# Performance work log

Hardware: AMD Instinct MI355X
Metric: run time of the kernel (lower is better)

The kernel has to match this reference:

```python
import jax, jax.numpy as jnp
import numpy as np

D_MODEL = 512
STATE = 128
HALF = STATE // 2
SEQ = 4096
BATCH = 8


def setup_inputs() -> dict:
    key = jax.random.key(0)
    ks = jax.random.split(key, 4)
    u = jax.random.normal(ks[0], (BATCH, SEQ, D_MODEL), dtype=jnp.float32)
    # HiPPO init: Lambda = -0.5 + i*pi*n, n=1..HALF
    n = jnp.arange(1, HALF + 1, dtype=jnp.float32)
    log_Lambda_real = jnp.log(jnp.full((HALF,), 0.5, dtype=jnp.float32))  # log(-real) with real=-0.5
    Lambda_imag = jnp.pi * n
    B_real = jnp.ones((HALF, D_MODEL), dtype=jnp.float32)
    B_imag = jnp.zeros((HALF, D_MODEL), dtype=jnp.float32)
    C_real = jax.random.normal(ks[1], (D_MODEL, HALF), dtype=jnp.float32) / np.sqrt(STATE)
    C_imag = jax.random.normal(ks[2], (D_MODEL, HALF), dtype=jnp.float32) / np.sqrt(STATE)
    D = jax.random.normal(ks[3], (D_MODEL, D_MODEL), dtype=jnp.float32) / np.sqrt(D_MODEL)
    log_Delta = jnp.array([-3.0], dtype=jnp.float32)
    return {
        "u": u,
        "log_Lambda_real": log_Lambda_real,
        "Lambda_imag": Lambda_imag,
        "B_real": B_real,
        "B_imag": B_imag,
        "C_real": C_real,
        "C_imag": C_imag,
        "D": D,
        "log_Delta": log_Delta,
    }


def reference(u, log_Lambda_real, Lambda_imag, B_real, B_imag, C_real, C_imag, D, log_Delta):
    T = u.shape[1]
    Bc = B_real + 1j * B_imag            # (N/2, P) complex
    Cc = C_real + 1j * C_imag            # (P, N/2) complex
    # --- bilinear (Tustin) discretization ---
    Delta = jnp.exp(log_Delta)           # (1,)
    Lambda = -jnp.exp(jnp.clip(log_Lambda_real, -10.0, 10.0)) + 1j * Lambda_imag  # (N/2,)
    denom = 1.0 - (Delta / 2.0) * Lambda
    A_bar = (1.0 + (Delta / 2.0) * Lambda) / denom          # (N/2,)
    B_bar = (Delta / denom)[:, None] * Bc                   # (N/2, P)
    # --- FFT convolution with the SSM kernel k[n,t] = A_bar[n]^t ---
    t_idx = jnp.arange(T)
    k = jnp.exp(jnp.log(A_bar)[:, None] * t_idx[None, :])   # (N/2, T)
    u_c = u.astype(jnp.complex64)
    v = jnp.einsum('np,btp->bnt', B_bar, u_c)               # (B, N/2, T)
    fft_size = 2 * T
    V_f = jnp.fft.fft(v, n=fft_size, axis=-1)
    K_f = jnp.fft.fft(k, n=fft_size, axis=-1)
    conv = jnp.fft.ifft(V_f * K_f[None, :, :], axis=-1)[..., :T]  # (B, N/2, T)
    y = 2.0 * jnp.einsum('pn,bnt->btp', Cc, conv).real      # (B, T, P)
    return y + u @ D.T
```

## Files before the change

### kernel.cpp

```cpp
#include <hip/hip_runtime.h>
#include <hip/hip_bf16.h>
#include <stdint.h>


#define BATCH 8
#define SEQ   4096
#define DMODEL 512
#define HALF  64
#define CHUNK 64
#define NCHUNK (SEQ / CHUNK)
#define NT    10

typedef __attribute__((ext_vector_type(8))) short short8;
typedef __attribute__((ext_vector_type(4))) float f32x4;

__device__ __forceinline__ unsigned short f2bf(float f) {
    unsigned int u = __float_as_uint(f);
    u += 0x7fffu + ((u >> 16) & 1u);
    return (unsigned short)(u >> 16);
}
__device__ __forceinline__ float bf2f(unsigned short s) {
    return __uint_as_float((unsigned)s << 16);
}

#define GLOAD_LDS16(g, l)                                                    \
    __builtin_amdgcn_global_load_lds(                                        \
        (const __attribute__((address_space(1))) unsigned int*)(g),          \
        (__attribute__((address_space(3))) unsigned int*)(l), 16, 0, 0)


__global__ void k_consts(const float* __restrict__ logLr,
                         const float* __restrict__ Li_in,
                         const float* __restrict__ logDelta,
                         float* __restrict__ sr, float* __restrict__ si,
                         float* __restrict__ ApR, float* __restrict__ ApI) {
    int n = threadIdx.x;
    float Delta = expf(logDelta[0]);
    float llr = fminf(fmaxf(logLr[n], -10.f), 10.f);
    float Lr = -expf(llr);
    float Li = Li_in[n];
    float dr = 1.f - 0.5f * Delta * Lr;
    float di = -0.5f * Delta * Li;
    float dn = dr * dr + di * di;
    float nr = 1.f + 0.5f * Delta * Lr;
    float ni = 0.5f * Delta * Li;
    float Ar = (nr * dr + ni * di) / dn;
    float Ai = (ni * dr - nr * di) / dn;
    sr[n] = Delta * dr / dn;
    si[n] = -Delta * di / dn;
    float pr = 1.f, pi = 0.f;
    for (int k = 0; k <= CHUNK; ++k) {
        ApR[k * HALF + n] = pr;
        ApI[k * HALF + n] = pi;
        float npr = pr * Ar - pi * Ai;
        float npi = pr * Ai + pi * Ar;
        pr = npr; pi = npi;
    }
}

__global__ void k_build_Mv(const float* __restrict__ Br, const float* __restrict__ Bi,
                           const float* __restrict__ sr, const float* __restrict__ si,
                           unsigned short* __restrict__ Mv) {
    int np = blockIdx.x, p = threadIdx.x;
    int n = np & 63;
    float br = Br[n * DMODEL + p], bi = Bi[n * DMODEL + p];
    float v = (np < HALF) ? (sr[n] * br - si[n] * bi)
                          : (si[n] * br + sr[n] * bi);
    Mv[np * DMODEL + p] = f2bf(v);
}

__global__ void k_build_W(const float* __restrict__ Cr, const float* __restrict__ Ci,
                          const float* __restrict__ D, unsigned short* __restrict__ W) {
    int p = blockIdx.x, j = threadIdx.x;
    float v;
    if (j < HALF) v = 2.f * Cr[p * HALF + j];
    else if (j < 2 * HALF) v = -2.f * Ci[p * HALF + (j - HALF)];
    else v = D[p * DMODEL + (j - 2 * HALF)];
    W[p * 640 + j] = f2bf(v);
}


__global__ void k_scanA(const unsigned short* __restrict__ Vb,
                        const float* __restrict__ ApR, const float* __restrict__ ApI,
                        float* __restrict__ E) {
    int tid = threadIdx.x;
    int n = tid & 63;
    int c = ((blockIdx.x & 31) << 1) + (tid >> 6);
    int b = blockIdx.x >> 5;
    float Ar = ApR[HALF + n], Ai = ApI[HALF + n];
    float xr = 0.f, xi = 0.f;
    size_t base = ((size_t)b * SEQ + (size_t)c * CHUNK) * 128 + n;
    for (int tl = 0; tl < CHUNK; ++tl) {
        float vr = bf2f(Vb[base]), vi = bf2f(Vb[base + 64]);
        float nxr = Ar * xr - Ai * xi + vr;
        float nxi = Ar * xi + Ai * xr + vi;
        xr = nxr; xi = nxi;
        base += 128;
    }
    int eidx = ((b * NCHUNK + c) * 2) * HALF + n;
    E[eidx] = xr; E[eidx + 64] = xi;
}

__global__ void k_scanB(const float* __restrict__ E, float* __restrict__ Carry,
                        const float* __restrict__ ApR, const float* __restrict__ ApI) {
    int lane = threadIdx.x & 63;
    int wv = threadIdx.x >> 6;
    int b = blockIdx.x;
    for (int n = wv; n < HALF; n += 8) {
        float wr = ApR[CHUNK * HALF + n], wi = ApI[CHUNK * HALF + n];
        int idx = ((b * NCHUNK + lane) * 2) * HALF + n;
        float sR = E[idx], sI = E[idx + 64];
#pragma unroll
        for (int s = 1; s < 64; s <<= 1) {
            float pR = __shfl_up(sR, s, 64);
            float pI = __shfl_up(sI, s, 64);
            if (lane >= s) {
                sR += wr * pR - wi * pI;
                sI += wr * pI + wi * pR;
            }
            float nwr = wr * wr - wi * wi;
            float nwi = 2.f * wr * wi;
            wr = nwr; wi = nwi;
        }
        float cR = __shfl_up(sR, 1, 64);
        float cI = __shfl_up(sI, 1, 64);
        if (lane == 0) { cR = 0.f; cI = 0.f; }
        Carry[idx] = cR; Carry[idx + 64] = cI;
    }
}

__global__ void k_scanC(const unsigned short* __restrict__ Vb,
                        const float* __restrict__ Carry,
                        const float* __restrict__ ApR, const float* __restrict__ ApI,
                        unsigned short* __restrict__ Xb) {
    int tid = threadIdx.x;
    int n = tid & 63;
    int c = ((blockIdx.x & 31) << 1) + (tid >> 6);
    int b = blockIdx.x >> 5;
    int cidx = ((b * NCHUNK + c) * 2) * HALF + n;
    float xr = Carry[cidx], xi = Carry[cidx + 64];
    float Ar = ApR[HALF + n], Ai = ApI[HALF + n];
    size_t base = ((size_t)b * SEQ + (size_t)c * CHUNK) * 128 + n;
    for (int tl = 0; tl < CHUNK; ++tl) {
        float vr = bf2f(Vb[base]), vi = bf2f(Vb[base + 64]);
        float nxr = Ar * xr - Ai * xi + vr;
        float nxi = Ar * xi + Ai * xr + vi;
        xr = nxr; xi = nxi;
        Xb[base] = f2bf(xr); Xb[base + 64] = f2bf(xi);
        base += 128;
    }
}

__global__ __launch_bounds__(512) void gemm1(const float* __restrict__ U,
                                             const unsigned short* __restrict__ Mv,
                                             unsigned short* __restrict__ Vb,
                                             unsigned short* __restrict__ Ub) {
    __shared__ __align__(16) unsigned short As[64 * 32];
    __shared__ __align__(16) unsigned short Bs[128 * 32];
    const int tid = threadIdx.x;
    const int lane = tid & 63;
    const int w = tid >> 6;
    const int wm = w >> 2, wn = w & 3;
    const int l15 = lane & 15, l4 = lane >> 4;
    const int row0 = blockIdx.x * 64;
    const int srow = tid >> 3;
    const int sh = (tid & 7) * 4;

    f32x4 acc[2][2];
#pragma unroll
    for (int m = 0; m < 2; ++m)
#pragma unroll
        for (int n = 0; n < 2; ++n) acc[m][n] = (f32x4)(0.f);

    for (int k0 = 0; k0 < DMODEL; k0 += 32) {
        const float4 av = *(const float4*)(U + (size_t)(row0 + srow) * DMODEL + k0 + sh);

        __syncthreads();

        GLOAD_LDS16(Mv + (size_t)(tid >> 2) * DMODEL + k0 + (tid & 3) * 8,
                    &Bs[(w * 64) * 8]);

        uint2 wa;
        wa.x = (unsigned)f2bf(av.x) | ((unsigned)f2bf(av.y) << 16);
        wa.y = (unsigned)f2bf(av.z) | ((unsigned)f2bf(av.w) << 16);
        *(uint2*)&As[srow * 32 + sh] = wa;
        *(uint2*)&Ub[(size_t)(row0 + srow) * DMODEL + k0 + sh] = wa;

        __syncthreads();

        short8 af[2], bf[2];
#pragma unroll
        for (int m = 0; m < 2; ++m)
            af[m] = *(const short8*)&As[(wm * 32 + m * 16 + l15) * 32 + l4 * 8];
#pragma unroll
        for (int n = 0; n < 2; ++n)
            bf[n] = *(const short8*)&Bs[(wn * 32 + n * 16 + l15) * 32 + l4 * 8];
#pragma unroll
        for (int m = 0; m < 2; ++m)
#pragma unroll
            for (int n = 0; n < 2; ++n)
                acc[m][n] = __builtin_amdgcn_mfma_f32_16x16x32_bf16(af[m], bf[n], acc[m][n], 0, 0, 0);
    }

#pragma unroll
    for (int m = 0; m < 2; ++m) {
        int rbase = row0 + wm * 32 + m * 16 + l4 * 4;
#pragma unroll
        for (int n = 0; n < 2; ++n) {
            int col = wn * 32 + n * 16 + l15;
#pragma unroll
            for (int r = 0; r < 4; ++r)
                Vb[(size_t)(rbase + r) * 128 + col] = f2bf(acc[m][n][r]);
        }
    }
}


#define STAGE_K(t, kh, j) do {                                                 \
    int c_ = (kh) * 1024 + (j) * 512 + tid;                                    \
    int ct_ = c_ ^ (((c_ >> 5) & 1) << 1);                                     \
    int r_ = (ct_ >> 2) & 255;                                                 \
    int kcol_ = (t) * 64 + (kh) * 32 + (ct_ & 3) * 8;                          \
    const unsigned short* asrc_ = (kcol_ < 128)                                \
        ? Xb + (size_t)(row0 + r_) * 128 + kcol_                               \
        : Ub + (size_t)(row0 + r_) * 512 + (kcol_ - 128);                      \
    GLOAD_LDS16(asrc_, &As[((t) & 1) * 16384 + ((kh) * 1024 + (j) * 512 + w * 64) * 8]); \
    GLOAD_LDS16(W + (size_t)(col0 + r_) * 640 + kcol_,                         \
                &Bs[((t) & 1) * 16384 + ((kh) * 1024 + (j) * 512 + w * 64) * 8]); \
} while (0)

#define LDAB(t, kh) do {                                                       \
    _Pragma("unroll") for (int i_ = 0; i_ < 8; ++i_) {                         \
        int r_ = wm * 128 + i_ * 16 + l15;                                     \
        int c_ = (l4 * 8) ^ (((r_ >> 3) & 1) << 4);                            \
        af[i_] = *(const short8*)&As[((t) & 1) * 16384 + (kh) * 8192 + r_ * 32 + c_]; \
    }                                                                          \
    _Pragma("unroll") for (int j_ = 0; j_ < 4; ++j_) {                         \
        int r_ = wn * 64 + j_ * 16 + l15;                                      \
        int c_ = (l4 * 8) ^ (((r_ >> 3) & 1) << 4);                            \
        bf[j_] = *(const short8*)&Bs[((t) & 1) * 16384 + (kh) * 8192 + r_ * 32 + c_]; \
    } } while (0)

#define MFMA32() do {                                                          \
    __builtin_amdgcn_s_setprio(1);                                             \
    _Pragma("unroll") for (int i_ = 0; i_ < 8; ++i_)                           \
    _Pragma("unroll") for (int j_ = 0; j_ < 4; ++j_)                           \
        acc[i_][j_] = __builtin_amdgcn_mfma_f32_16x16x32_bf16(                 \
            af[i_], bf[j_], acc[i_][j_], 0, 0, 0);                             \
    __builtin_amdgcn_s_setprio(0);                                             \
} while (0)

#define PHASE_SYNC(N) do {                                                     \
    asm volatile("s_waitcnt vmcnt(" #N ")" ::: "memory");                      \
    __builtin_amdgcn_s_barrier();                                              \
    __builtin_amdgcn_sched_barrier(0);                                         \
} while (0)

__global__ __launch_bounds__(512) void gemm23_8p(const unsigned short* __restrict__ Xb,
                                                 const unsigned short* __restrict__ Ub,
                                                 const unsigned short* __restrict__ W,
                                                 float* __restrict__ C) {
    __shared__ __align__(16) unsigned short As[2 * 16384];
    __shared__ __align__(16) unsigned short Bs[2 * 16384];
    const int tid = threadIdx.x;
    const int lane = tid & 63;
    const int w = tid >> 6;
    const int wm = w >> 2, wn = w & 3;
    const int l15 = lane & 15, l4 = lane >> 4;

    int lin = blockIdx.y * gridDim.x + blockIdx.x;
    int sw = (lin & 7) * 32 + (lin >> 3);
    const int row0 = (sw & 127) * 256;
    const int col0 = (sw >> 7) * 256;

    f32x4 acc[8][4];
#pragma unroll
    for (int m = 0; m < 8; ++m)
#pragma unroll
        for (int n = 0; n < 4; ++n) acc[m][n] = (f32x4)(0.f);

    STAGE_K(0, 0, 0); STAGE_K(0, 0, 1);
    STAGE_K(0, 1, 0); STAGE_K(0, 1, 1);
    STAGE_K(1, 0, 0); STAGE_K(1, 0, 1);

    short8 af[8], bf[4];
    for (int t = 0; t < NT - 1; ++t) {
        PHASE_SYNC(8);
        LDAB(t, 0);
        STAGE_K(t + 1, 1, 0); STAGE_K(t + 1, 1, 1);
        MFMA32();
        PHASE_SYNC(8);
        LDAB(t, 1);
        if (t < NT - 2) { STAGE_K(t + 2, 0, 0); STAGE_K(t + 2, 0, 1); }
        MFMA32();
    }
    PHASE_SYNC(4);
    LDAB(NT - 1, 0);
    MFMA32();
    PHASE_SYNC(0);
    LDAB(NT - 1, 1);
    MFMA32();

#pragma unroll
    for (int m = 0; m < 8; ++m) {
        int rbase = row0 + wm * 128 + m * 16 + l4 * 4;
#pragma unroll
        for (int n = 0; n < 4; ++n) {
            int col = col0 + wn * 64 + n * 16 + l15;
#pragma unroll
            for (int r = 0; r < 4; ++r)
                C[(size_t)(rbase + r) * DMODEL + col] = acc[m][n][r];
        }
    }
}


extern "C" void kernel_launch(void* const* d_in, const int* in_sizes, int n_in,
                              void* d_out, int out_size, void* d_ws, size_t ws_size,
                              hipStream_t stream) {
    const float* u      = (const float*)d_in[0];
    const float* logLr  = (const float*)d_in[1];
    const float* Li     = (const float*)d_in[2];
    const float* Br     = (const float*)d_in[3];
    const float* Bi     = (const float*)d_in[4];
    const float* Cr     = (const float*)d_in[5];
    const float* Ci     = (const float*)d_in[6];
    const float* D      = (const float*)d_in[7];
    const float* logDel = (const float*)d_in[8];
    float* out = (float*)d_out;

    const size_t M = (size_t)BATCH * SEQ;
    unsigned short* Vb = (unsigned short*)d_ws;
    unsigned short* Ub = Vb + M * 128;
    unsigned short* Xb = Ub + M * 512;
    unsigned short* Mv = Xb + M * 128;
    unsigned short* W  = Mv + 128 * 512;
    float* fp    = (float*)(W + 512 * 640);
    float* E     = fp;
    float* Carry = E + 65536;
    float* ApR   = Carry + 65536;
    float* ApI   = ApR + 4160;
    float* sr    = ApI + 4160;
    float* si    = sr + 64;

    hipLaunchKernelGGL(k_consts, dim3(1), dim3(64), 0, stream,
                       logLr, Li, logDel, sr, si, ApR, ApI);
    hipLaunchKernelGGL(k_build_Mv, dim3(128), dim3(512), 0, stream, Br, Bi, sr, si, Mv);
    hipLaunchKernelGGL(k_build_W, dim3(512), dim3(640), 0, stream, Cr, Ci, D, W);

    hipLaunchKernelGGL(gemm1, dim3(M / 64), dim3(512), 0, stream, u, Mv, Vb, Ub);

    hipLaunchKernelGGL(k_scanA, dim3(256), dim3(128), 0, stream, Vb, ApR, ApI, E);
    hipLaunchKernelGGL(k_scanB, dim3(BATCH), dim3(512), 0, stream, E, Carry, ApR, ApI);
    hipLaunchKernelGGL(k_scanC, dim3(256), dim3(128), 0, stream, Vb, Carry, ApR, ApI, Xb);

    hipLaunchKernelGGL(gemm23_8p, dim3(M / 256, DMODEL / 256), dim3(512), 0, stream,
                       Xb, Ub, W, out);
}
```

Before: 85.56 us.

## Fuse local chunk scan into gemm1, make scanC carry-only, retile final GEMM

The first GEMM now stages its output tile in LDS, runs the per-chunk intra-chunk scan there, writes the locally scanned Vb plus chunk end states, and drops the separate scanA kernel. scanC no longer runs a serial recurrence; it adds the carry times precomputed powers of A to the already-scanned values. The final GEMM moves to 128x256 tiles with a 3-stage LDS ring, a vmcnt-based pipeline and a coalesced LDS-staged float4 epilogue. The scan inside gemm1 runs serially on a single wave while the other waves wait, and the ApR/ApI power table must hold A^1..A^64 for the carry formula to be correct.

```diff
diff --git a/kernel.cpp b/kernel.cpp
--- a/kernel.cpp
+++ b/kernel.cpp
@@ -9,7 +9,6 @@
 #define HALF  64
 #define CHUNK 64
 #define NCHUNK (SEQ / CHUNK)
-#define NT    10
 
 typedef __attribute__((ext_vector_type(8))) short short8;
 typedef __attribute__((ext_vector_type(4))) float f32x4;
@@ -79,26 +78,101 @@
     W[p * 640 + j] = f2bf(v);
 }
 
-
-__global__ void k_scanA(const unsigned short* __restrict__ Vb,
-                        const float* __restrict__ ApR, const float* __restrict__ ApI,
-                        float* __restrict__ E) {
-    int tid = threadIdx.x;
-    int n = tid & 63;
-    int c = ((blockIdx.x & 31) << 1) + (tid >> 6);
-    int b = blockIdx.x >> 5;
-    float Ar = ApR[HALF + n], Ai = ApI[HALF + n];
-    float xr = 0.f, xi = 0.f;
-    size_t base = ((size_t)b * SEQ + (size_t)c * CHUNK) * 128 + n;
-    for (int tl = 0; tl < CHUNK; ++tl) {
-        float vr = bf2f(Vb[base]), vi = bf2f(Vb[base + 64]);
-        float nxr = Ar * xr - Ai * xi + vr;
-        float nxi = Ar * xi + Ai * xr + vi;
-        xr = nxr; xi = nxi;
-        base += 128;
-    }
-    int eidx = ((b * NCHUNK + c) * 2) * HALF + n;
-    E[eidx] = xr; E[eidx + 64] = xi;
+__global__ __launch_bounds__(512) void gemm1(const float* __restrict__ U,
+                                             const unsigned short* __restrict__ Mv,
+                                             unsigned short* __restrict__ Vb,
+                                             unsigned short* __restrict__ Ub,
+                                             const float* __restrict__ ApR,
+                                             const float* __restrict__ ApI,
+                                             float* __restrict__ E) {
+    __shared__ __align__(16) unsigned short As[64 * 32];
+    __shared__ __align__(16) unsigned short Bs[128 * 32];
+    __shared__ __align__(16) float Vt[64 * 132];
+    const int tid = threadIdx.x;
+    const int lane = tid & 63;
+    const int w = tid >> 6;
+    const int wm = w >> 2, wn = w & 3;
+    const int l15 = lane & 15, l4 = lane >> 4;
+    const int row0 = blockIdx.x * 64;
+    const int srow = tid >> 3;
+    const int sh = (tid & 7) * 4;
+
+    f32x4 acc[2][2];
+#pragma unroll
+    for (int m = 0; m < 2; ++m)
+#pragma unroll
+        for (int n = 0; n < 2; ++n) acc[m][n] = (f32x4)(0.f);
+
+    for (int k0 = 0; k0 < DMODEL; k0 += 32) {
+        const float4 av = *(const float4*)(U + (size_t)(row0 + srow) * DMODEL + k0 + sh);
+
+        __syncthreads();
+
+        GLOAD_LDS16(Mv + (size_t)(tid >> 2) * DMODEL + k0 + (tid & 3) * 8,
+                    &Bs[(w * 64) * 8]);
+
+        uint2 wa;
+        wa.x = (unsigned)f2bf(av.x) | ((unsigned)f2bf(av.y) << 16);
+        wa.y = (unsigned)f2bf(av.z) | ((unsigned)f2bf(av.w) << 16);
+        *(uint2*)&As[srow * 32 + sh] = wa;
+        *(uint2*)&Ub[(size_t)(row0 + srow) * DMODEL + k0 + sh] = wa;
+
+        __syncthreads();
+
+        short8 af[2], bf[2];
+#pragma unroll
+        for (int m = 0; m < 2; ++m)
+            af[m] = *(const short8*)&As[(wm * 32 + m * 16 + l15) * 32 + l4 * 8];
+#pragma unroll
+        for (int n = 0; n < 2; ++n)
+            bf[n] = *(const short8*)&Bs[(wn * 32 + n * 16 + l15) * 32 + l4 * 8];
+#pragma unroll
+        for (int m = 0; m < 2; ++m)
+#pragma unroll
+            for (int n = 0; n < 2; ++n)
+                acc[m][n] = __builtin_amdgcn_mfma_f32_16x16x32_bf16(af[m], bf[n], acc[m][n], 0, 0, 0);
+    }
+
+    __syncthreads();
+#pragma unroll
+    for (int m = 0; m < 2; ++m)
+#pragma unroll
+        for (int n = 0; n < 2; ++n)
+#pragma unroll
+            for (int r = 0; r < 4; ++r)
+                Vt[(wm * 32 + m * 16 + l4 * 4 + r) * 132 + wn * 32 + n * 16 + l15] = acc[m][n][r];
+    __syncthreads();
+
+    const int b = row0 >> 12;
+    const int c = (row0 >> 6) & 63;
+    if (tid < 64) {
+        int n = tid;
+        float Ar = ApR[HALF + n], Ai = ApI[HALF + n];
+        float xr = 0.f, xi = 0.f;
+        for (int tl = 0; tl < CHUNK; ++tl) {
+            float vr = Vt[tl * 132 + n], vi = Vt[tl * 132 + 64 + n];
+            float nxr = Ar * xr - Ai * xi + vr;
+            float nxi = Ar * xi + Ai * xr + vi;
+            xr = nxr; xi = nxi;
+            Vt[tl * 132 + n] = xr; Vt[tl * 132 + 64 + n] = xi;
+        }
+        int ei = ((b * NCHUNK + c) * 2) * HALF + n;
+        E[ei] = xr; E[ei + 64] = xi;
+    }
+    __syncthreads();
+
+#pragma unroll
+    for (int j = 0; j < 2; ++j) {
+        int idx = tid * 2 + j;
+        int row = idx >> 4, oc = idx & 15;
+        const float* vs = &Vt[row * 132 + oc * 8];
+        uint4 pk;
+        pk.x = (unsigned)f2bf(vs[0]) | ((unsigned)f2bf(vs[1]) << 16);
+        pk.y = (unsigned)f2bf(vs[2]) | ((unsigned)f2bf(vs[3]) << 16);
+        pk.z = (unsigned)f2bf(vs[4]) | ((unsigned)f2bf(vs[5]) << 16);
+        pk.w = (unsigned)f2bf(vs[6]) | ((unsigned)f2bf(vs[7]) << 16);
+        *(uint4*)&Vb[(size_t)(row0 + row) * 128 + oc * 8] = pk;
+    }
 }
 
 __global__ void k_scanB(const float* __restrict__ E, float* __restrict__ Carry,
@@ -138,178 +212,113 @@
     int c = ((blockIdx.x & 31) << 1) + (tid >> 6);
     int b = blockIdx.x >> 5;
     int cidx = ((b * NCHUNK + c) * 2) * HALF + n;
-    float xr = Carry[cidx], xi = Carry[cidx + 64];
-    float Ar = ApR[HALF + n], Ai = ApI[HALF + n];
+    float cr = Carry[cidx], ci = Carry[cidx + 64];
     size_t base = ((size_t)b * SEQ + (size_t)c * CHUNK) * 128 + n;
     for (int tl = 0; tl < CHUNK; ++tl) {
-        float vr = bf2f(Vb[base]), vi = bf2f(Vb[base + 64]);
-        float nxr = Ar * xr - Ai * xi + vr;
-        float nxi = Ar * xi + Ai * xr + vi;
-        xr = nxr; xi = nxi;
+        float pr = ApR[(tl + 1) * HALF + n], pi = ApI[(tl + 1) * HALF + n];
+        float xr = bf2f(Vb[base])      + pr * cr - pi * ci;
+        float xi = bf2f(Vb[base + 64]) + pr * ci + pi * cr;
         Xb[base] = f2bf(xr); Xb[base + 64] = f2bf(xi);
         base += 128;
     }
 }
 
-__global__ __launch_bounds__(512) void gemm1(const float* __restrict__ U,
-                                             const unsigned short* __restrict__ Mv,
-                                             unsigned short* __restrict__ Vb,
-                                             unsigned short* __restrict__ Ub) {
-    __shared__ __align__(16) unsigned short As[64 * 32];
-    __shared__ __align__(16) unsigned short Bs[128 * 32];
+
+#define STAGE_P(p) do {                                                        \
+    const int kb_ = ((p) >> 1) * 64 + ((p) & 1) * 32;                          \
+    { int c_ = tid; int ct_ = c_ ^ (((c_ >> 5) & 1) << 1);                     \
+      int r_ = ct_ >> 2; int kc_ = kb_ + (ct_ & 3) * 8;                        \
+      const unsigned short* s_ = (kc_ < 128)                                   \
+          ? Xb + (size_t)(row0 + r_) * 128 + kc_                               \
+          : Ub + (size_t)(row0 + r_) * 512 + (kc_ - 128);                      \
+      GLOAD_LDS16(s_, &lds[((p) % 3) * 4096 + (w * 64) * 8]); }                \
+    _Pragma("unroll") for (int j_ = 0; j_ < 2; ++j_) {                         \
+      int c_ = j_ * 512 + tid; int ct_ = c_ ^ (((c_ >> 5) & 1) << 1);          \
+      int r_ = ct_ >> 2; int kc_ = kb_ + (ct_ & 3) * 8;                        \
+      GLOAD_LDS16(W + (size_t)(col0 + r_) * 640 + kc_,                         \
+                  &lds[12288 + ((p) % 3) * 8192 + (j_ * 512 + w * 64) * 8]);   \
+    } } while (0)
+
+#define LDAB_P(p) do {                                                         \
+    _Pragma("unroll") for (int i_ = 0; i_ < 4; ++i_) {                         \
+        int r_ = wm * 64 + i_ * 16 + l15;                                      \
+        int c_ = (l4 * 8) ^ (((r_ >> 3) & 1) << 4);                            \
+        af[i_] = *(const short8*)&lds[((p) % 3) * 4096 + r_ * 32 + c_]; }      \
+    _Pragma("unroll") for (int j_ = 0; j_ < 4; ++j_) {                         \
+        int r_ = wn * 64 + j_ * 16 + l15;                                      \
+        int c_ = (l4 * 8) ^ (((r_ >> 3) & 1) << 4);                            \
+        bf[j_] = *(const short8*)&lds[12288 + ((p) % 3) * 8192 + r_ * 32 + c_]; } \
+    } while (0)
+
+#define MFMA16() do {                                                          \
+    __builtin_amdgcn_s_setprio(1);                                             \
+    _Pragma("unroll") for (int i_ = 0; i_ < 4; ++i_)                           \
+    _Pragma("unroll") for (int j_ = 0; j_ < 4; ++j_)                           \
+        acc[i_][j_] = __builtin_amdgcn_mfma_f32_16x16x32_bf16(                 \
+            af[i_], bf[j_], acc[i_][j_], 0, 0, 0);                             \
+    __builtin_amdgcn_s_setprio(0);                                             \
+} while (0)
+
+__global__ __launch_bounds__(512) void gemm23_r(const unsigned short* __restrict__ Xb,
+                                                const unsigned short* __restrict__ Ub,
+                                                const unsigned short* __restrict__ W,
+                                                float* __restrict__ C) {
+    __shared__ __align__(16) unsigned short lds[36864];
     const int tid = threadIdx.x;
     const int lane = tid & 63;
     const int w = tid >> 6;
     const int wm = w >> 2, wn = w & 3;
     const int l15 = lane & 15, l4 = lane >> 4;
-    const int row0 = blockIdx.x * 64;
-    const int srow = tid >> 3;
-    const int sh = (tid & 7) * 4;
-
-    f32x4 acc[2][2];
-#pragma unroll
-    for (int m = 0; m < 2; ++m)
-#pragma unroll
-        for (int n = 0; n < 2; ++n) acc[m][n] = (f32x4)(0.f);
-
-    for (int k0 = 0; k0 < DMODEL; k0 += 32) {
-        const float4 av = *(const float4*)(U + (size_t)(row0 + srow) * DMODEL + k0 + sh);
-
+
+    int lin = blockIdx.y * gridDim.x + blockIdx.x;
+    int sw = (lin & 7) * 64 + (lin >> 3);
+    const int row0 = (sw & 255) * 128;
+    const int col0 = (sw >> 8) * 256;
+
+    f32x4 acc[4][4];
+#pragma unroll
+    for (int m = 0; m < 4; ++m)
+#pragma unroll
+        for (int n = 0; n < 4; ++n) acc[m][n] = (f32x4)(0.f);
+
+    STAGE_P(0);
+    STAGE_P(1);
+
+    short8 af[4], bf[4];
+#pragma unroll
+    for (int p = 0; p < 19; ++p) {
+        asm volatile("s_waitcnt vmcnt(3)" ::: "memory");
+        __builtin_amdgcn_s_barrier();
+        __builtin_amdgcn_sched_barrier(0);
+        LDAB_P(p);
+        if (p < 18) STAGE_P(p + 2);
+        MFMA16();
+    }
+    asm volatile("s_waitcnt vmcnt(0)" ::: "memory");
+    __builtin_amdgcn_s_barrier();
+    __builtin_amdgcn_sched_barrier(0);
+    LDAB_P(19);
+    MFMA16();
+
+    float* lf = (float*)lds;
+#pragma unroll
+    for (int i = 0; i < 4; ++i) {
         __syncthreads();
-
-        GLOAD_LDS16(Mv + (size_t)(tid >> 2) * DMODEL + k0 + (tid & 3) * 8,
-                    &Bs[(w * 64) * 8]);
-
-        uint2 wa;
-        wa.x = (unsigned)f2bf(av.x) | ((unsigned)f2bf(av.y) << 16);
-        wa.y = (unsigned)f2bf(av.z) | ((unsigned)f2bf(av.w) << 16);
-        *(uint2*)&As[srow * 32 + sh] = wa;
-        *(uint2*)&Ub[(size_t)(row0 + srow) * DMODEL + k0 + sh] = wa;
-
+#pragma unroll
+        for (int j = 0; j < 4; ++j)
+#pragma unroll
+            for (int r = 0; r < 4; ++r)
+                lf[(wm * 16 + l4 * 4 + r) * 264 + wn * 64 + j * 16 + l15] = acc[i][j][r];
         __syncthreads();
-
-        short8 af[2], bf[2];
-#pragma unroll
-        for (int m = 0; m < 2; ++m)
-            af[m] = *(const short8*)&As[(wm * 32 + m * 16 + l15) * 32 + l4 * 8];
-#pragma unroll
-        for (int n = 0; n < 2; ++n)
-            bf[n] = *(const short8*)&Bs[(wn * 32 + n * 16 + l15) * 32 + l4 * 8];
-#pragma unroll
-        for (int m = 0; m < 2; ++m)
-#pragma unroll
-            for (int n = 0; n < 2; ++n)
-                acc[m][n] = __builtin_amdgcn_mfma_f32_16x16x32_bf16(af[m], bf[n], acc[m][n], 0, 0, 0);
-    }
-
-#pragma unroll
-    for (int m = 0; m < 2; ++m) {
-        int rbase = row0 + wm * 32 + m * 16 + l4 * 4;
-#pragma unroll
-        for (int n = 0; n < 2; ++n) {
-            int col = wn * 32 + n * 16 + l15;
-#pragma unroll
-            for (int r = 0; r < 4; ++r)
-                Vb[(size_t)(rbase + r) * 128 + col] = f2bf(acc[m][n][r]);
-        }
-    }
-}
-
-
-#define STAGE_K(t, kh, j) do {                                                 \
-    int c_ = (kh) * 1024 + (j) * 512 + tid;                                    \
-    int ct_ = c_ ^ (((c_ >> 5) & 1) << 1);                                     \
-    int r_ = (ct_ >> 2) & 255;                                                 \
-    int kcol_ = (t) * 64 + (kh) * 32 + (ct_ & 3) * 8;                          \
-    const unsigned short* asrc_ = (kcol_ < 128)                                \
-        ? Xb + (size_t)(row0 + r_) * 128 + kcol_                               \
-        : Ub + (size_t)(row0 + r_) * 512 + (kcol_ - 128);                      \
-    GLOAD_LDS16(asrc_, &As[((t) & 1) * 16384 + ((kh) * 1024 + (j) * 512 + w * 64) * 8]); \
-    GLOAD_LDS16(W + (size_t)(col0 + r_) * 640 + kcol_,                         \
-                &Bs[((t) & 1) * 16384 + ((kh) * 1024 + (j) * 512 + w * 64) * 8]); \
-} while (0)
-
-#define LDAB(t, kh) do {                                                       \
-    _Pragma("unroll") for (int i_ = 0; i_ < 8; ++i_) {                         \
-        int r_ = wm * 128 + i_ * 16 + l15;                                     \
-        int c_ = (l4 * 8) ^ (((r_ >> 3) & 1) << 4);                            \
-        af[i_] = *(const short8*)&As[((t) & 1) * 16384 + (kh) * 8192 + r_ * 32 + c_]; \
-    }                                                                          \
-    _Pragma("unroll") for (int j_ = 0; j_ < 4; ++j_) {                         \
-        int r_ = wn * 64 + j_ * 16 + l15;                                      \
-        int c_ = (l4 * 8) ^ (((r_ >> 3) & 1) << 4);                            \
-        bf[j_] = *(const short8*)&Bs[((t) & 1) * 16384 + (kh) * 8192 + r_ * 32 + c_]; \
-    } } while (0)
-
-#define MFMA32() do {                                                          \
-    __builtin_amdgcn_s_setprio(1);                                             \
-    _Pragma("unroll") for (int i_ = 0; i_ < 8; ++i_)                           \
-    _Pragma("unroll") for (int j_ = 0; j_ < 4; ++j_)                           \
-        acc[i_][j_] = __builtin_amdgcn_mfma_f32_16x16x32_bf16(                 \
-            af[i_], bf[j_], acc[i_][j_], 0, 0, 0);                             \
-    __builtin_amdgcn_s_setprio(0);                                             \
-} while (0)
-
-#define PHASE_SYNC(N) do {                                                     \
-    asm volatile("s_waitcnt vmcnt(" #N ")" ::: "memory");                      \
-    __builtin_amdgcn_s_barrier();                                              \
-    __builtin_amdgcn_sched_barrier(0);                                         \
-} while (0)
-
-__global__ __launch_bounds__(512) void gemm23_8p(const unsigned short* __restrict__ Xb,
-                                                 const unsigned short* __restrict__ Ub,
-                                                 const unsigned short* __restrict__ W,
-                                                 float* __restrict__ C) {
-    __shared__ __align__(16) unsigned short As[2 * 16384];
-    __shared__ __align__(16) unsigned short Bs[2 * 16384];
-    const int tid = threadIdx.x;
-    const int lane = tid & 63;
-    const int w = tid >> 6;
-    const int wm = w >> 2, wn = w & 3;
-    const int l15 = lane & 15, l4 = lane >> 4;
-
-    int lin = blockIdx.y * gridDim.x + blockIdx.x;
-    int sw = (lin & 7) * 32 + (lin >> 3);
-    const int row0 = (sw & 127) * 256;
-    const int col0 = (sw >> 7) * 256;
-
-    f32x4 acc[8][4];
-#pragma unroll
-    for (int m = 0; m < 8; ++m)
-#pragma unroll
-        for (int n = 0; n < 4; ++n) acc[m][n] = (f32x4)(0.f);
-
-    STAGE_K(0, 0, 0); STAGE_K(0, 0, 1);
-    STAGE_K(0, 1, 0); STAGE_K(0, 1, 1);
-    STAGE_K(1, 0, 0); STAGE_K(1, 0, 1);
-
-    short8 af[8], bf[4];
-    for (int t = 0; t < NT - 1; ++t) {
-        PHASE_SYNC(8);
-        LDAB(t, 0);
-        STAGE_K(t + 1, 1, 0); STAGE_K(t + 1, 1, 1);
-        MFMA32();
-        PHASE_SYNC(8);
-        LDAB(t, 1);
-        if (t < NT - 2) { STAGE_K(t + 2, 0, 0); STAGE_K(t + 2, 0, 1); }
-        MFMA32();
-    }
-    PHASE_SYNC(4);
-    LDAB(NT - 1, 0);
-    MFMA32();
-    PHASE_SYNC(0);
-    LDAB(NT - 1, 1);
-    MFMA32();
-
-#pragma unroll
-    for (int m = 0; m < 8; ++m) {
-        int rbase = row0 + wm * 128 + m * 16 + l4 * 4;
-#pragma unroll
-        for (int n = 0; n < 4; ++n) {
-            int col = col0 + wn * 64 + n * 16 + l15;
-#pragma unroll
-            for (int r = 0; r < 4; ++r)
-                C[(size_t)(rbase + r) * DMODEL + col] = acc[m][n][r];
+        {
+            int rr = tid >> 4;
+            int cg = tid & 15;
+            int gr = row0 + (rr >> 4) * 64 + i * 16 + (rr & 15);
+            float* cp = &C[(size_t)gr * DMODEL + col0 + cg * 16];
+            const float* ls = &lf[rr * 264 + cg * 16];
+#pragma unroll
+            for (int j = 0; j < 4; ++j)
+                *(float4*)(cp + j * 4) = *(const float4*)(ls + j * 4);
         }
     }
 }
@@ -348,12 +357,12 @@
     hipLaunchKernelGGL(k_build_Mv, dim3(128), dim3(512), 0, stream, Br, Bi, sr, si, Mv);
     hipLaunchKernelGGL(k_build_W, dim3(512), dim3(640), 0, stream, Cr, Ci, D, W);
 
-    hipLaunchKernelGGL(gemm1, dim3(M / 64), dim3(512), 0, stream, u, Mv, Vb, Ub);
-
-    hipLaunchKernelGGL(k_scanA, dim3(256), dim3(128), 0, stream, Vb, ApR, ApI, E);
+    hipLaunchKernelGGL(gemm1, dim3(M / 64), dim3(512), 0, stream,
+                       u, Mv, Vb, Ub, ApR, ApI, E);
+
     hipLaunchKernelGGL(k_scanB, dim3(BATCH), dim3(512), 0, stream, E, Carry, ApR, ApI);
     hipLaunchKernelGGL(k_scanC, dim3(256), dim3(128), 0, stream, Vb, Carry, ApR, ApI, Xb);
 
-    hipLaunchKernelGGL(gemm23_8p, dim3(M / 256, DMODEL / 256), dim3(512), 0, stream,
+    hipLaunchKernelGGL(gemm23_r, dim3(M / 128, DMODEL / 256), dim3(512), 0, stream,
                        Xb, Ub, W, out);
 }
```

Result: slower. 105.4 us (+23.2%).

## Replace four-slot K pipeline with simple two-stage double buffer in output GEMM

Applied to the files above, without the earlier changes.

Restructures the final fused GEMM's main loop. The old schedule staged 32-wide K halves into four LDS slots with partial vmcnt waits, so loads stayed in flight across phases. The new one runs 20 uniform phases over a two-slot double buffer: wait for all loads, barrier, issue the next phase's loads, then read LDS and run the MFMAs. This halves LDS use and simplifies control flow, but leaves only one phase of prefetch in flight, so global-load latency is hidden less.

```diff
diff --git a/kernel.cpp b/kernel.cpp
--- a/kernel.cpp
+++ b/kernel.cpp
@@ -9,7 +9,7 @@
 #define HALF  64
 #define CHUNK 64
 #define NCHUNK (SEQ / CHUNK)
-#define NT    10
+#define NPH   20
 
 typedef __attribute__((ext_vector_type(8))) short short8;
 typedef __attribute__((ext_vector_type(4))) float f32x4;
@@ -216,30 +216,32 @@
 }
 
 
-#define STAGE_K(t, kh, j) do {                                                 \
-    int c_ = (kh) * 1024 + (j) * 512 + tid;                                    \
-    int ct_ = c_ ^ (((c_ >> 5) & 1) << 1);                                     \
-    int r_ = (ct_ >> 2) & 255;                                                 \
-    int kcol_ = (t) * 64 + (kh) * 32 + (ct_ & 3) * 8;                          \
-    const unsigned short* asrc_ = (kcol_ < 128)                                \
-        ? Xb + (size_t)(row0 + r_) * 128 + kcol_                               \
-        : Ub + (size_t)(row0 + r_) * 512 + (kcol_ - 128);                      \
-    GLOAD_LDS16(asrc_, &As[((t) & 1) * 16384 + ((kh) * 1024 + (j) * 512 + w * 64) * 8]); \
-    GLOAD_LDS16(W + (size_t)(col0 + r_) * 640 + kcol_,                         \
-                &Bs[((t) & 1) * 16384 + ((kh) * 1024 + (j) * 512 + w * 64) * 8]); \
-} while (0)
-
-#define LDAB(t, kh) do {                                                       \
+#define STAGE_P(p) do {                                                        \
+    const int t_ = (p) >> 1, kh_ = (p) & 1, s_ = (p) & 1;                      \
+    _Pragma("unroll") for (int j_ = 0; j_ < 2; ++j_) {                         \
+        int c_ = j_ * 512 + tid;                                               \
+        int ct_ = c_ ^ (((c_ >> 5) & 1) << 1);                                 \
+        int r_ = (ct_ >> 2) & 255;                                             \
+        int kcol_ = t_ * 64 + kh_ * 32 + (ct_ & 3) * 8;                        \
+        const unsigned short* asrc_ = (kcol_ < 128)                            \
+            ? Xb + (size_t)(row0 + r_) * 128 + kcol_                           \
+            : Ub + (size_t)(row0 + r_) * 512 + (kcol_ - 128);                  \
+        GLOAD_LDS16(asrc_, &As[s_ * 8192 + (j_ * 512 + w * 64) * 8]);          \
+        GLOAD_LDS16(W + (size_t)(col0 + r_) * 640 + kcol_,                     \
+                    &Bs[s_ * 8192 + (j_ * 512 + w * 64) * 8]);                 \
+    } } while (0)
+
+#define LDAB_P(p) do {                                                         \
+    const int s_ = (p) & 1;                                                    \
     _Pragma("unroll") for (int i_ = 0; i_ < 8; ++i_) {                         \
         int r_ = wm * 128 + i_ * 16 + l15;                                     \
         int c_ = (l4 * 8) ^ (((r_ >> 3) & 1) << 4);                            \
-        af[i_] = *(const short8*)&As[((t) & 1) * 16384 + (kh) * 8192 + r_ * 32 + c_]; \
-    }                                                                          \
+        af[i_] = *(const short8*)&As[s_ * 8192 + r_ * 32 + c_]; }              \
     _Pragma("unroll") for (int j_ = 0; j_ < 4; ++j_) {                         \
         int r_ = wn * 64 + j_ * 16 + l15;                                      \
         int c_ = (l4 * 8) ^ (((r_ >> 3) & 1) << 4);                            \
-        bf[j_] = *(const short8*)&Bs[((t) & 1) * 16384 + (kh) * 8192 + r_ * 32 + c_]; \
-    } } while (0)
+        bf[j_] = *(const short8*)&Bs[s_ * 8192 + r_ * 32 + c_]; }              \
+    } while (0)
 
 #define MFMA32() do {                                                          \
     __builtin_amdgcn_s_setprio(1);                                             \
@@ -250,18 +252,12 @@
     __builtin_amdgcn_s_setprio(0);                                             \
 } while (0)
 
-#define PHASE_SYNC(N) do {                                                     \
-    asm volatile("s_waitcnt vmcnt(" #N ")" ::: "memory");                      \
-    __builtin_amdgcn_s_barrier();                                              \
-    __builtin_amdgcn_sched_barrier(0);                                         \
-} while (0)
-
-__global__ __launch_bounds__(512) void gemm23_8p(const unsigned short* __restrict__ Xb,
+__global__ __launch_bounds__(512) void gemm23_2s(const unsigned short* __restrict__ Xb,
                                                  const unsigned short* __restrict__ Ub,
                                                  const unsigned short* __restrict__ W,
                                                  float* __restrict__ C) {
-    __shared__ __align__(16) unsigned short As[2 * 16384];
-    __shared__ __align__(16) unsigned short Bs[2 * 16384];
+    __shared__ __align__(16) unsigned short As[2 * 8192];
+    __shared__ __align__(16) unsigned short Bs[2 * 8192];
     const int tid = threadIdx.x;
     const int lane = tid & 63;
     const int w = tid >> 6;
@@ -279,27 +275,18 @@
 #pragma unroll
         for (int n = 0; n < 4; ++n) acc[m][n] = (f32x4)(0.f);
 
-    STAGE_K(0, 0, 0); STAGE_K(0, 0, 1);
-    STAGE_K(0, 1, 0); STAGE_K(0, 1, 1);
-    STAGE_K(1, 0, 0); STAGE_K(1, 0, 1);
+    STAGE_P(0);
 
     short8 af[8], bf[4];
-    for (int t = 0; t < NT - 1; ++t) {
-        PHASE_SYNC(8);
-        LDAB(t, 0);
-        STAGE_K(t + 1, 1, 0); STAGE_K(t + 1, 1, 1);
+#pragma unroll 2
+    for (int p = 0; p < NPH; ++p) {
+        asm volatile("s_waitcnt vmcnt(0)" ::: "memory");
+        __builtin_amdgcn_s_barrier();
+        __builtin_amdgcn_sched_barrier(0);
+        if (p < NPH - 1) STAGE_P(p + 1);
+        LDAB_P(p);
         MFMA32();
-        PHASE_SYNC(8);
-        LDAB(t, 1);
-        if (t < NT - 2) { STAGE_K(t + 2, 0, 0); STAGE_K(t + 2, 0, 1); }
-        MFMA32();
-    }
-    PHASE_SYNC(4);
-    LDAB(NT - 1, 0);
-    MFMA32();
-    PHASE_SYNC(0);
-    LDAB(NT - 1, 1);
-    MFMA32();
+    }
 
 #pragma unroll
     for (int m = 0; m < 8; ++m) {
@@ -354,6 +341,6 @@
     hipLaunchKernelGGL(k_scanB, dim3(BATCH), dim3(512), 0, stream, E, Carry, ApR, ApI);
     hipLaunchKernelGGL(k_scanC, dim3(256), dim3(128), 0, stream, Vb, Carry, ApR, ApI, Xb);
 
-    hipLaunchKernelGGL(gemm23_8p, dim3(M / 256, DMODEL / 256), dim3(512), 0, stream,
+    hipLaunchKernelGGL(gemm23_2s, dim3(M / 256, DMODEL / 256), dim3(512), 0, stream,
                        Xb, Ub, W, out);
 }
```

After: 92.42 us. 8.0% more time.

## Merge setup kernels, compute poles inline, fold carry scan into final scan

Applied to the files above, without the earlier changes.

Merges k_consts, k_build_Mv and k_build_W into one k_build launch. The per-chunk pole A is now recomputed inside each scan kernel, so the power table is no longer needed. The separate carry-propagation kernel k_scanB is removed: each chunk in k_scanCB sums the end states of all earlier chunks, weighted by powers of A^64. This cuts the pipeline from seven launches to four, at the cost of O(c) redundant serial work per chunk (up to 63 iterations) and possibly different rounding.

```diff
diff --git a/kernel.cpp b/kernel.cpp
--- a/kernel.cpp
+++ b/kernel.cpp
@@ -23,18 +23,9 @@
     return __uint_as_float((unsigned)s << 16);
 }
 
-#define GLOAD_LDS16(g, l)                                                    \
-    __builtin_amdgcn_global_load_lds(                                        \
-        (const __attribute__((address_space(1))) unsigned int*)(g),          \
-        (__attribute__((address_space(3))) unsigned int*)(l), 16, 0, 0)
-
-
-__global__ void k_consts(const float* __restrict__ logLr,
-                         const float* __restrict__ Li_in,
-                         const float* __restrict__ logDelta,
-                         float* __restrict__ sr, float* __restrict__ si,
-                         float* __restrict__ ApR, float* __restrict__ ApI) {
-    int n = threadIdx.x;
+__device__ __forceinline__ void poleA(const float* logLr, const float* Li_in,
+                                      const float* logDelta, int n,
+                                      float& Ar, float& Ai) {
     float Delta = expf(logDelta[0]);
     float llr = fminf(fmaxf(logLr[n], -10.f), 10.f);
     float Lr = -expf(llr);
@@ -44,50 +35,59 @@
     float dn = dr * dr + di * di;
     float nr = 1.f + 0.5f * Delta * Lr;
     float ni = 0.5f * Delta * Li;
-    float Ar = (nr * dr + ni * di) / dn;
-    float Ai = (ni * dr - nr * di) / dn;
-    sr[n] = Delta * dr / dn;
-    si[n] = -Delta * di / dn;
-    float pr = 1.f, pi = 0.f;
-    for (int k = 0; k <= CHUNK; ++k) {
-        ApR[k * HALF + n] = pr;
-        ApI[k * HALF + n] = pi;
-        float npr = pr * Ar - pi * Ai;
-        float npi = pr * Ai + pi * Ar;
-        pr = npr; pi = npi;
-    }
-}
-
-__global__ void k_build_Mv(const float* __restrict__ Br, const float* __restrict__ Bi,
-                           const float* __restrict__ sr, const float* __restrict__ si,
-                           unsigned short* __restrict__ Mv) {
-    int np = blockIdx.x, p = threadIdx.x;
-    int n = np & 63;
-    float br = Br[n * DMODEL + p], bi = Bi[n * DMODEL + p];
-    float v = (np < HALF) ? (sr[n] * br - si[n] * bi)
-                          : (si[n] * br + sr[n] * bi);
-    Mv[np * DMODEL + p] = f2bf(v);
-}
-
-__global__ void k_build_W(const float* __restrict__ Cr, const float* __restrict__ Ci,
-                          const float* __restrict__ D, unsigned short* __restrict__ W) {
-    int p = blockIdx.x, j = threadIdx.x;
-    float v;
-    if (j < HALF) v = 2.f * Cr[p * HALF + j];
-    else if (j < 2 * HALF) v = -2.f * Ci[p * HALF + (j - HALF)];
-    else v = D[p * DMODEL + (j - 2 * HALF)];
-    W[p * 640 + j] = f2bf(v);
-}
-
+    Ar = (nr * dr + ni * di) / dn;
+    Ai = (ni * dr - nr * di) / dn;
+}
+
+#define GLOAD_LDS16(g, l)                                                    \
+    __builtin_amdgcn_global_load_lds(                                        \
+        (const __attribute__((address_space(1))) unsigned int*)(g),          \
+        (__attribute__((address_space(3))) unsigned int*)(l), 16, 0, 0)
+
+__global__ void k_build(const float* __restrict__ logLr, const float* __restrict__ Li_in,
+                        const float* __restrict__ logDelta,
+                        const float* __restrict__ Br, const float* __restrict__ Bi,
+                        const float* __restrict__ Cr, const float* __restrict__ Ci,
+                        const float* __restrict__ D,
+                        unsigned short* __restrict__ Mv, unsigned short* __restrict__ W) {
+    int bid = blockIdx.x;
+    if (bid < 128) {
+        int np = bid, p = threadIdx.x;
+        if (p < DMODEL) {
+            int n = np & 63;
+            float Delta = expf(logDelta[0]);
+            float llr = fminf(fmaxf(logLr[n], -10.f), 10.f);
+            float Lr = -expf(llr);
+            float Li = Li_in[n];
+            float dr = 1.f - 0.5f * Delta * Lr;
+            float di = -0.5f * Delta * Li;
+            float dn = dr * dr + di * di;
+            float sr = Delta * dr / dn;
+            float si = -Delta * di / dn;
+            float br = Br[n * DMODEL + p], bi = Bi[n * DMODEL + p];
+            float v = (np < HALF) ? (sr * br - si * bi) : (si * br + sr * bi);
+            Mv[np * DMODEL + p] = f2bf(v);
+        }
+    } else {
+        int p = bid - 128, j = threadIdx.x;
+        float v;
+        if (j < HALF) v = 2.f * Cr[p * HALF + j];
+        else if (j < 2 * HALF) v = -2.f * Ci[p * HALF + (j - HALF)];
+        else v = D[p * DMODEL + (j - 2 * HALF)];
+        W[p * 640 + j] = f2bf(v);
+    }
+}
 
 __global__ void k_scanA(const unsigned short* __restrict__ Vb,
-                        const float* __restrict__ ApR, const float* __restrict__ ApI,
+                        const float* __restrict__ logLr, const float* __restrict__ Li_in,
+                        const float* __restrict__ logDelta,
                         float* __restrict__ E) {
     int tid = threadIdx.x;
     int n = tid & 63;
     int c = ((blockIdx.x & 31) << 1) + (tid >> 6);
     int b = blockIdx.x >> 5;
-    float Ar = ApR[HALF + n], Ai = ApI[HALF + n];
+    float Ar, Ai;
+    poleA(logLr, Li_in, logDelta, n, Ar, Ai);
     float xr = 0.f, xi = 0.f;
     size_t base = ((size_t)b * SEQ + (size_t)c * CHUNK) * 128 + n;
     for (int tl = 0; tl < CHUNK; ++tl) {
@@ -101,45 +101,34 @@
     E[eidx] = xr; E[eidx + 64] = xi;
 }
 
-__global__ void k_scanB(const float* __restrict__ E, float* __restrict__ Carry,
-                        const float* __restrict__ ApR, const float* __restrict__ ApI) {
-    int lane = threadIdx.x & 63;
-    int wv = threadIdx.x >> 6;
-    int b = blockIdx.x;
-    for (int n = wv; n < HALF; n += 8) {
-        float wr = ApR[CHUNK * HALF + n], wi = ApI[CHUNK * HALF + n];
-        int idx = ((b * NCHUNK + lane) * 2) * HALF + n;
-        float sR = E[idx], sI = E[idx + 64];
-#pragma unroll
-        for (int s = 1; s < 64; s <<= 1) {
-            float pR = __shfl_up(sR, s, 64);
-            float pI = __shfl_up(sI, s, 64);
-            if (lane >= s) {
-                sR += wr * pR - wi * pI;
-                sI += wr * pI + wi * pR;
-            }
-            float nwr = wr * wr - wi * wi;
-            float nwi = 2.f * wr * wi;
-            wr = nwr; wi = nwi;
-        }
-        float cR = __shfl_up(sR, 1, 64);
-        float cI = __shfl_up(sI, 1, 64);
-        if (lane == 0) { cR = 0.f; cI = 0.f; }
-        Carry[idx] = cR; Carry[idx + 64] = cI;
-    }
-}
-
-__global__ void k_scanC(const unsigned short* __restrict__ Vb,
-                        const float* __restrict__ Carry,
-                        const float* __restrict__ ApR, const float* __restrict__ ApI,
-                        unsigned short* __restrict__ Xb) {
+__global__ void k_scanCB(const unsigned short* __restrict__ Vb,
+                         const float* __restrict__ E,
+                         const float* __restrict__ logLr, const float* __restrict__ Li_in,
+                         const float* __restrict__ logDelta,
+                         unsigned short* __restrict__ Xb) {
     int tid = threadIdx.x;
     int n = tid & 63;
     int c = ((blockIdx.x & 31) << 1) + (tid >> 6);
     int b = blockIdx.x >> 5;
-    int cidx = ((b * NCHUNK + c) * 2) * HALF + n;
-    float xr = Carry[cidx], xi = Carry[cidx + 64];
-    float Ar = ApR[HALF + n], Ai = ApI[HALF + n];
+    float Ar, Ai;
+    poleA(logLr, Li_in, logDelta, n, Ar, Ai);
+    float a64r = Ar, a64i = Ai;
+#pragma unroll
+    for (int s = 0; s < 6; ++s) {
+        float t = a64r * a64r - a64i * a64i;
+        a64i = 2.f * a64r * a64i;
+        a64r = t;
+    }
+    float xr = 0.f, xi = 0.f, wr = 1.f, wi = 0.f;
+    for (int jj = 1; jj <= c; ++jj) {
+        int ei = ((b * NCHUNK + (c - jj)) * 2) * HALF + n;
+        float er = E[ei], ev = E[ei + 64];
+        xr += wr * er - wi * ev;
+        xi += wr * ev + wi * er;
+        float nwr = wr * a64r - wi * a64i;
+        float nwi = wr * a64i + wi * a64r;
+        wr = nwr; wi = nwi;
+    }
     size_t base = ((size_t)b * SEQ + (size_t)c * CHUNK) * 128 + n;
     for (int tl = 0; tl < CHUNK; ++tl) {
         float vr = bf2f(Vb[base]), vi = bf2f(Vb[base + 64]);
@@ -335,24 +324,17 @@
     unsigned short* Xb = Ub + M * 512;
     unsigned short* Mv = Xb + M * 128;
     unsigned short* W  = Mv + 128 * 512;
-    float* fp    = (float*)(W + 512 * 640);
-    float* E     = fp;
-    float* Carry = E + 65536;
-    float* ApR   = Carry + 65536;
-    float* ApI   = ApR + 4160;
-    float* sr    = ApI + 4160;
-    float* si    = sr + 64;
-
-    hipLaunchKernelGGL(k_consts, dim3(1), dim3(64), 0, stream,
-                       logLr, Li, logDel, sr, si, ApR, ApI);
-    hipLaunchKernelGGL(k_build_Mv, dim3(128), dim3(512), 0, stream, Br, Bi, sr, si, Mv);
-    hipLaunchKernelGGL(k_build_W, dim3(512), dim3(640), 0, stream, Cr, Ci, D, W);
+    float* E     = (float*)(W + 512 * 640);
+
+    hipLaunchKernelGGL(k_build, dim3(640), dim3(640), 0, stream,
+                       logLr, Li, logDel, Br, Bi, Cr, Ci, D, Mv, W);
 
     hipLaunchKernelGGL(gemm1, dim3(M / 64), dim3(512), 0, stream, u, Mv, Vb, Ub);
 
-    hipLaunchKernelGGL(k_scanA, dim3(256), dim3(128), 0, stream, Vb, ApR, ApI, E);
-    hipLaunchKernelGGL(k_scanB, dim3(BATCH), dim3(512), 0, stream, E, Carry, ApR, ApI);
-    hipLaunchKernelGGL(k_scanC, dim3(256), dim3(128), 0, stream, Vb, Carry, ApR, ApI, Xb);
+    hipLaunchKernelGGL(k_scanA, dim3(256), dim3(128), 0, stream,
+                       Vb, logLr, Li, logDel, E);
+    hipLaunchKernelGGL(k_scanCB, dim3(256), dim3(128), 0, stream,
+                       Vb, E, logLr, Li, logDel, Xb);
 
     hipLaunchKernelGGL(gemm23_8p, dim3(M / 256, DMODEL / 256), dim3(512), 0, stream,
                        Xb, Ub, W, out);
```

Result: faster. 79.39 us (-7.2%).
